# Kernel tuning notes

Hardware: AMD Instinct MI355X
Metric: run time of the kernel (lower is better)

The kernel has to match this reference:

```python
import jax, jax.numpy as jnp
import numpy as np

B = 1024
D = 128  # in_out_dim


def _lin(k, i, o):
    return jax.random.normal(k, (i, o), jnp.float32) / np.sqrt(i)


def setup_inputs() -> dict:
    key = jax.random.key(0)
    ks = jax.random.split(key, 24)
    inp = {
        'pseudo_t': jax.random.uniform(ks[0], (), jnp.float32),
        'x': jax.random.normal(ks[1], (B, D), jnp.float32),
        'g_x': jax.random.normal(ks[2], (B, 1), jnp.float32),
        'p': jax.random.uniform(ks[3], (B, 1), jnp.float32),
        # GRN encoder: 128->1024->960->896 (Tanh), decoder 896->128
        'gw0': _lin(ks[4], 128, 1024), 'gb0': jnp.zeros((1024,), jnp.float32),
        'gw1': _lin(ks[5], 1024, 960), 'gb1': jnp.zeros((960,), jnp.float32),
        'gw2': _lin(ks[6], 960, 896), 'gb2': jnp.zeros((896,), jnp.float32),
        'gdw': _lin(ks[7], 896, 128), 'gdb': jnp.zeros((128,), jnp.float32),
        # BRD encoder: 129->512->448 (Tanh), decoder 448->1
        'bw0': _lin(ks[8], 129, 512), 'bb0': jnp.zeros((512,), jnp.float32),
        'bw1': _lin(ks[9], 512, 448), 'bb1': jnp.zeros((448,), jnp.float32),
        'bdw': _lin(ks[10], 448, 1), 'bdb': jnp.zeros((1,), jnp.float32),
    }
    return inp


def reference(pseudo_t, x, g_x, p, gw0, gb0, gw1, gb1, gw2, gb2, gdw, gdb,
              bw0, bb0, bw1, bb1, bdw, bdb):
    bsz = x.shape[0]
    x_gene = x[:, :-1]                       # [B, D-1]
    s = jnp.full((bsz, 1), pseudo_t, x.dtype)

    def grn(state):                          # [..., D] -> [..., D]
        h = jnp.tanh(state @ gw0 + gb0)
        h = jnp.tanh(h @ gw1 + gb1)
        h = jnp.tanh(h @ gw2 + gb2)
        return h @ gdw + gdb

    dx_dt = grn(jnp.concatenate([s, x_gene], axis=1))   # [B, D]

    # BRD growth function g(x, t)
    st = jnp.concatenate([s, x], axis=1)                # [B, D+1]
    e = jnp.tanh(st @ bw0 + bb0)
    e = jnp.tanh(e @ bw1 + bb1)
    g = e @ bdw + bdb                                   # [B, 1]

    # trace of d(dx_dt[:, :D-1]) / d(x_gene), per sample (CNF divergence)
    s_scalar = jnp.reshape(pseudo_t, (1,)).astype(x.dtype)

    def f_single(xg_i):                                 # [D-1] -> [D]
        return grn(jnp.concatenate([s_scalar, xg_i]))

    jac = jax.vmap(jax.jacfwd(f_single))(x_gene)        # [B, D, D-1]
    tr = jnp.trace(jac[:, :D - 1, :], axis1=1, axis2=2) # [B]

    dp_dt = g - p * tr[:, None]                         # [B, 1]
    return (dx_dt, g, dp_dt)
```

## Files before the change

### kernel.cpp

```cpp
#include <hip/hip_runtime.h>


typedef __bf16 bf16;
typedef __bf16 bf16x8 __attribute__((ext_vector_type(8)));
typedef float floatx4 __attribute__((ext_vector_type(4)));

#if defined(__has_builtin)
#if __has_builtin(__builtin_amdgcn_global_load_lds)
#define HAVE_GLL 1
#endif
#endif

typedef __attribute__((address_space(3))) char lds_char_t;
typedef __attribute__((address_space(1))) const char gbl_char_t;

__device__ inline void async_load16(const void* gp, void* lp) {
#ifdef HAVE_GLL
  __builtin_amdgcn_global_load_lds((gbl_char_t*)gp, (lds_char_t*)lp, 16, 0, 0);
#else
  *(bf16x8*)lp = *(const bf16x8*)gp;
#endif
}

__device__ inline void stage_async(const bf16* src, long row0, int ld, int kc,
                                   bf16* dst, int wid, int sr8, int cph) {
#pragma unroll
  for (int t = 0; t < 4; ++t) {
    const int r = (wid * 4 + t) * 8 + sr8;
    const int csrc = (cph - r) & 7;
    async_load16(src + (row0 + r) * (size_t)ld + kc + csrc * 8,
                 dst + r * 64 + cph * 8);
  }
}

__device__ inline void mfma_block(const bf16* As, const bf16* Bs,
                                  floatx4 (&acc)[4][4], int wm, int wn,
                                  int l16, int quad) {
#pragma unroll
  for (int ks = 0; ks < 2; ++ks) {
    bf16x8 af[4], bfv[4];
#pragma unroll
    for (int mt = 0; mt < 4; ++mt) {
      const int r = wm * 64 + mt * 16 + l16;
      const int c = (ks * 4 + quad + r) & 7;
      af[mt] = *(const bf16x8*)(As + r * 64 + c * 8);
    }
#pragma unroll
    for (int nt = 0; nt < 4; ++nt) {
      const int r = wn * 64 + nt * 16 + l16;
      const int c = (ks * 4 + quad + r) & 7;
      bfv[nt] = *(const bf16x8*)(Bs + r * 64 + c * 8);
    }
#pragma unroll
    for (int mt = 0; mt < 4; ++mt)
#pragma unroll
      for (int nt = 0; nt < 4; ++nt)
        acc[mt][nt] = __builtin_amdgcn_mfma_f32_16x16x32_bf16(af[mt], bfv[nt], acc[mt][nt], 0, 0, 0);
  }
}

struct TArgs {
  const bf16* A;
  const bf16* B;
  const bf16* d1b;
  bf16* Upr;
  const bf16* d2b;
  const float* gdw;
  float* tr;
  int i0; int K; int ch;
};

template <int MODE>
__global__ __launch_bounds__(256, 4) void kt_tile(TArgs p) {
  const int idx = blockIdx.x;
  const int mt8 = (idx >> 3) & 7;
  const int nb  = ((idx >> 6) << 3) + (idx & 7);
  if (nb >= p.ch) return;
  if (MODE == 1 && mt8 == 7) return;

  __shared__ __align__(16) char lds[34816];
  bf16* As = (bf16*)lds;
  bf16* Bs = As + 8192;
  bf16* bounce = (bf16*)lds;
  __shared__ float red4[4];

  const int tid  = threadIdx.x;
  const int wid  = tid >> 6, lane = tid & 63;
  const int wm   = wid & 1, wn = wid >> 1;
  const int quad = lane >> 4, l16 = lane & 15;
  const int sr8  = lane >> 3, cph = lane & 7;
  const int m0   = mt8 * 128;
  const int ig   = p.i0 + nb;
  const int n0   = nb * 128;

  floatx4 acc[4][4];
#pragma unroll
  for (int a = 0; a < 4; ++a)
#pragma unroll
    for (int b = 0; b < 4; ++b)
#pragma unroll
      for (int r = 0; r < 4; ++r) acc[a][b][r] = 0.0f;

  for (int kc = 0; kc < p.K; kc += 64) {
    stage_async(p.A, m0, 1024, kc, As, wid, sr8, cph);
    stage_async(p.B, n0, 1024, kc, Bs, wid, sr8, cph);
    __syncthreads();
    mfma_block(As, Bs, acc, wm, wn, l16, quad);
    __syncthreads();
  }

  if (MODE == 0) {
#pragma unroll
    for (int nt = 0; nt < 4; ++nt) {
      const int nl = wn * 64 + nt * 16 + l16;
#pragma unroll
      for (int mt = 0; mt < 4; ++mt)
#pragma unroll
        for (int r = 0; r < 4; ++r) {
          const int ml = wm * 64 + mt * 16 + quad * 4 + r;
          const int mg = m0 + ml;
          const float d1v = (mg < 960) ? (float)p.d1b[(size_t)ig * 960 + mg] : 0.0f;
          bounce[nl * 136 + ml] = (bf16)(acc[mt][nt][r] * d1v);
        }
    }
    __syncthreads();
    const int r2 = tid >> 1, half16 = tid & 1;
#pragma unroll
    for (int c = 0; c < 8; ++c) {
      const int ch16 = half16 * 8 + c;
      bf16x8 v = *(const bf16x8*)(bounce + r2 * 136 + ch16 * 8);
      *(bf16x8*)(p.Upr + (size_t)(n0 + r2) * 1024 + m0 + ch16 * 8) = v;
    }
  } else {
    float s = 0.0f;
#pragma unroll
    for (int nt = 0; nt < 4; ++nt) {
      const int d = wn * 64 + nt * 16 + l16;
      if (d < 127) {
#pragma unroll
        for (int mt = 0; mt < 4; ++mt)
#pragma unroll
          for (int r = 0; r < 4; ++r) {
            const int mg = m0 + wm * 64 + mt * 16 + quad * 4 + r;
            const float w = (float)p.d2b[(size_t)ig * 896 + mg] * p.gdw[mg * 128 + d];
            s += acc[mt][nt][r] * w;
          }
      }
    }
#pragma unroll
    for (int off = 1; off < 64; off <<= 1) s += __shfl_xor(s, off, 64);
    if (lane == 0) red4[wid] = s;
    __syncthreads();
    if (tid == 0) atomicAdd(p.tr + ig, red4[0] + red4[1] + red4[2] + red4[3]);
  }
}

struct FArgs {
  const bf16* A; int lda;
  const bf16* Bt; int ldb;
  const float* bias;
  bf16* C; int ldc;
  bf16* D; int ldd;
  float* outF; int ldo;
  int K; int realN;
};

template <int ACT>
__global__ __launch_bounds__(256) void kt_fwd(FArgs p) {
  __shared__ __align__(16) bf16 As[8192];
  __shared__ __align__(16) bf16 Bs[8192];
  const int tid  = threadIdx.x;
  const int wid  = tid >> 6, lane = tid & 63;
  const int wm   = wid & 1, wn = wid >> 1;
  const int quad = lane >> 4, l16 = lane & 15;
  const int sr8  = lane >> 3, cph = lane & 7;
  const int m0   = blockIdx.x * 128;
  const int bn0  = blockIdx.y * 128;

  floatx4 acc[4][4];
#pragma unroll
  for (int a = 0; a < 4; ++a)
#pragma unroll
    for (int b = 0; b < 4; ++b)
#pragma unroll
      for (int r = 0; r < 4; ++r) acc[a][b][r] = 0.0f;

  for (int kc = 0; kc < p.K; kc += 64) {
    stage_async(p.A, m0, p.lda, kc, As, wid, sr8, cph);
    stage_async(p.Bt, bn0, p.ldb, kc, Bs, wid, sr8, cph);
    __syncthreads();
    mfma_block(As, Bs, acc, wm, wn, l16, quad);
    __syncthreads();
  }

#pragma unroll
  for (int nt = 0; nt < 4; ++nt) {
    const int ng = bn0 + wn * 64 + nt * 16 + l16;
    const float bv = (ng < p.realN) ? p.bias[ng] : 0.0f;
#pragma unroll
    for (int mt = 0; mt < 4; ++mt)
#pragma unroll
      for (int r = 0; r < 4; ++r) {
        const int i = m0 + wm * 64 + mt * 16 + quad * 4 + r;
        const float v = acc[mt][nt][r] + bv;
        if (ACT) {
          const float t = tanhf(v);
          p.C[(size_t)i * p.ldc + ng] = (ng < p.realN) ? (bf16)t : (bf16)0.0f;
          if (p.D && ng < p.realN)
            p.D[(size_t)i * p.ldd + ng] = (bf16)(1.0f - t * t);
        } else if (ng < p.realN) {
          p.outF[(size_t)i * p.ldo + ng] = v;
        }
      }
  }
}

struct PArgs {
  const float *gw0, *gw1, *gw2, *gdw, *bw0, *bw1, *pt, *x;
  bf16 *gw0b, *gw0t, *gw1t, *gw2t, *gdwt, *bw0t, *bw1t, *Xg, *Xb;
};

__device__ inline void tpose_tile(bf16* dst, const float* src, int R, int C,
                                  int ldd, int tile, int tilesX, float* tl,
                                  int tid) {
  const int r0 = (tile % tilesX) * 64;
  const int c0 = (tile / tilesX) * 64;
  const int tx = tid & 63, ty0 = tid >> 6;
#pragma unroll
  for (int i = 0; i < 16; ++i) {
    const int ty = ty0 + i * 4;
    const int r = r0 + ty, c = c0 + tx;
    tl[ty * 65 + tx] = (r < R && c < C) ? src[(size_t)r * C + c] : 0.0f;
  }
  __syncthreads();
#pragma unroll
  for (int i = 0; i < 16; ++i) {
    const int ty = ty0 + i * 4;
    dst[(size_t)(c0 + ty) * ldd + r0 + tx] = (bf16)tl[tx * 65 + ty];
  }
}

__global__ __launch_bounds__(256) void kt_prep(PArgs p) {
  __shared__ float tl[64 * 65];
  int b = blockIdx.x;
  const int t = threadIdx.x;
  if (b < 512) { p.gw0b[b * 256 + t] = (bf16)p.gw0[b * 256 + t]; return; }
  b -= 512;
  if (b < 768) {
    const int idx = b * 256 + t;
    const int i = idx / 192, c = idx % 192;
    const float s = p.pt[0];
    float vb;
    if (c == 0) vb = s;
    else if (c <= 128) vb = p.x[i * 128 + c - 1];
    else vb = 0.0f;
    p.Xb[i * 192 + c] = (bf16)vb;
    if (c < 128) p.Xg[i * 128 + c] = (bf16)((c == 0) ? s : p.x[i * 128 + c - 1]);
    return;
  }
  b -= 768;
  if (b < 32)  { tpose_tile(p.gw0t, p.gw0, 128, 1024, 128, b, 2, tl, t);  return; }
  b -= 32;
  if (b < 256) { tpose_tile(p.gw1t, p.gw1, 1024, 960, 1024, b, 16, tl, t); return; }
  b -= 256;
  if (b < 256) { tpose_tile(p.gw2t, p.gw2, 960, 896, 1024, b, 16, tl, t); return; }
  b -= 256;
  if (b < 32)  { tpose_tile(p.gdwt, p.gdw, 896, 128, 1024, b, 16, tl, t); return; }
  b -= 32;
  if (b < 24)  { tpose_tile(p.bw0t, p.bw0, 129, 512, 192, b, 3, tl, t);  return; }
  b -= 24;
  if (b < 64)  { tpose_tile(p.bw1t, p.bw1, 512, 448, 512, b, 8, tl, t);  return; }
}

__global__ __launch_bounds__(256) void kt_g0(bf16* G0, const bf16* gw0b,
                                             const bf16* d0b, int i0, int ch) {
  const int b = blockIdx.x;
  const int nb = ((b >> 9) << 3) + (b & 7);
  const int inner = (b >> 3) & 63;
  if (nb >= ch) return;
  const int e = inner * 256 + threadIdx.x;
  const int d = e >> 7;
  const int j = (e & 127) << 3;
  const int ig = i0 + nb;
  const int wsel = (d + 1 < 128) ? d + 1 : 127;
  bf16x8 gv = *(const bf16x8*)(gw0b + wsel * 1024 + j);
  bf16x8 dv = *(const bf16x8*)(d0b + (size_t)ig * 1024 + j);
  bf16x8 v;
#pragma unroll
  for (int k = 0; k < 8; ++k) v[k] = (bf16)((float)gv[k] * (float)dv[k]);
  *(bf16x8*)(G0 + ((size_t)nb * 128 + d) * 1024 + j) = v;
}

__global__ __launch_bounds__(256) void kt_gdot(const bf16* e1b, const float* bdw,
                                               const float* bdb, float* gf, float* gout) {
  const int i = blockIdx.x * 4 + (threadIdx.x >> 6);
  const int lane = threadIdx.x & 63;
  float s = 0.0f;
  for (int k = lane; k < 448; k += 64) s += (float)e1b[(size_t)i * 512 + k] * bdw[k];
#pragma unroll
  for (int off = 32; off > 0; off >>= 1) s += __shfl_down(s, off, 64);
  if (lane == 0) {
    const float v = s + bdb[0];
    gf[i] = v;
    gout[i] = v;
  }
}

__global__ __launch_bounds__(256) void kt_fin(const float* gf, const float* tr,
                                              const float* pp, float* dp) {
  const int i = blockIdx.x * 256 + threadIdx.x;
  if (i < 1024) dp[i] = gf[i] - pp[i] * tr[i];
}

extern "C" void kernel_launch(void* const* d_in, const int* in_sizes, int n_in,
                              void* d_out, int out_size, void* d_ws, size_t ws_size,
                              hipStream_t stream) {
  const float* pt  = (const float*)d_in[0];
  const float* x   = (const float*)d_in[1];
  const float* pp  = (const float*)d_in[3];
  const float* gw0 = (const float*)d_in[4];
  const float* gb0 = (const float*)d_in[5];
  const float* gw1 = (const float*)d_in[6];
  const float* gb1 = (const float*)d_in[7];
  const float* gw2 = (const float*)d_in[8];
  const float* gb2 = (const float*)d_in[9];
  const float* gdw = (const float*)d_in[10];
  const float* gdb = (const float*)d_in[11];
  const float* bw0 = (const float*)d_in[12];
  const float* bb0 = (const float*)d_in[13];
  const float* bw1 = (const float*)d_in[14];
  const float* bb1 = (const float*)d_in[15];
  const float* bdw = (const float*)d_in[16];
  const float* bdb = (const float*)d_in[17];
  float* out = (float*)d_out;

  char* w = (char*)d_ws;
  size_t used = 0;
  auto alloc = [&](size_t nbytes) -> void* {
    void* r = w + used;
    used += (nbytes + 255) & ~(size_t)255;
    return r;
  };
  bf16* gw0b = (bf16*)alloc((size_t)128 * 1024 * 2);
  bf16* gw0t = (bf16*)alloc((size_t)1024 * 128 * 2);
  bf16* gw1t = (bf16*)alloc((size_t)1024 * 1024 * 2);
  bf16* gw2t = (bf16*)alloc((size_t)1024 * 1024 * 2);
  bf16* gdwt = (bf16*)alloc((size_t)128 * 1024 * 2);
  bf16* bw0t = (bf16*)alloc((size_t)512 * 192 * 2);
  bf16* bw1t = (bf16*)alloc((size_t)512 * 512 * 2);
  bf16* Xg   = (bf16*)alloc((size_t)1024 * 128 * 2);
  bf16* Xb   = (bf16*)alloc((size_t)1024 * 192 * 2);
  bf16* h0b  = (bf16*)alloc((size_t)1024 * 1024 * 2);
  bf16* h1b  = (bf16*)alloc((size_t)1024 * 1024 * 2);
  bf16* h2b  = (bf16*)alloc((size_t)1024 * 1024 * 2);
  bf16* e0b  = (bf16*)alloc((size_t)1024 * 512 * 2);
  bf16* e1b  = (bf16*)alloc((size_t)1024 * 512 * 2);
  bf16* d0b  = (bf16*)alloc((size_t)1024 * 1024 * 2);
  bf16* d1b  = (bf16*)alloc((size_t)1024 * 960 * 2);
  bf16* d2b  = (bf16*)alloc((size_t)1024 * 896 * 2);
  float* gf  = (float*)alloc(1024 * 4);
  float* tr  = (float*)alloc(1024 * 4);

  const size_t perSample = (size_t)128 * 1024 * 2;
  size_t avail = (ws_size > used) ? ws_size - used : 0;
  int CH = (int)(avail / (2 * perSample));
  if (CH > 256) CH = 256;
  if (CH < 1) CH = 1;
  bf16* G0  = (bf16*)alloc((size_t)CH * perSample);
  bf16* Upr = (bf16*)(w + used);

  hipMemsetAsync(tr, 0, 1024 * 4, stream);

  {
    PArgs a{gw0, gw1, gw2, gdw, bw0, bw1, pt, x,
            gw0b, gw0t, gw1t, gw2t, gdwt, bw0t, bw1t, Xg, Xb};
    kt_prep<<<dim3(1944), 256, 0, stream>>>(a);
  }

  {
    FArgs a{}; a.A = Xg; a.lda = 128; a.Bt = gw0t; a.ldb = 128; a.bias = gb0;
    a.C = h0b; a.ldc = 1024; a.D = d0b; a.ldd = 1024; a.K = 128; a.realN = 1024;
    kt_fwd<1><<<dim3(8, 8), 256, 0, stream>>>(a);
  }
  {
    FArgs a{}; a.A = h0b; a.lda = 1024; a.Bt = gw1t; a.ldb = 1024; a.bias = gb1;
    a.C = h1b; a.ldc = 1024; a.D = d1b; a.ldd = 960; a.K = 1024; a.realN = 960;
    kt_fwd<1><<<dim3(8, 8), 256, 0, stream>>>(a);
  }
  {
    FArgs a{}; a.A = h1b; a.lda = 1024; a.Bt = gw2t; a.ldb = 1024; a.bias = gb2;
    a.C = h2b; a.ldc = 1024; a.D = d2b; a.ldd = 896; a.K = 1024; a.realN = 896;
    kt_fwd<1><<<dim3(8, 7), 256, 0, stream>>>(a);
  }
  {
    FArgs a{}; a.A = h2b; a.lda = 1024; a.Bt = gdwt; a.ldb = 1024; a.bias = gdb;
    a.outF = out; a.ldo = 128; a.K = 896; a.realN = 128;
    kt_fwd<0><<<dim3(8, 1), 256, 0, stream>>>(a);
  }
  {
    FArgs a{}; a.A = Xb; a.lda = 192; a.Bt = bw0t; a.ldb = 192; a.bias = bb0;
    a.C = e0b; a.ldc = 512; a.K = 192; a.realN = 512;
    kt_fwd<1><<<dim3(8, 4), 256, 0, stream>>>(a);
  }
  {
    FArgs a{}; a.A = e0b; a.lda = 512; a.Bt = bw1t; a.ldb = 512; a.bias = bb1;
    a.C = e1b; a.ldc = 512; a.K = 512; a.realN = 448;
    kt_fwd<1><<<dim3(8, 4), 256, 0, stream>>>(a);
  }
  kt_gdot<<<dim3(256), 256, 0, stream>>>(e1b, bdw, bdb, gf, out + 131072);

  for (int i0 = 0; i0 < 1024; i0 += CH) {
    const int ch = (1024 - i0 < CH) ? (1024 - i0) : CH;
    const int ch8 = (ch + 7) & ~7;
    kt_g0<<<dim3(ch8 * 64), 256, 0, stream>>>(G0, gw0b, d0b, i0, ch);
    {
      TArgs a{}; a.A = gw1t; a.B = G0; a.d1b = d1b; a.Upr = Upr; a.i0 = i0;
      a.K = 1024; a.ch = ch;
      kt_tile<0><<<dim3(8 * ch8), 256, 0, stream>>>(a);
    }
    {
      TArgs a{}; a.A = gw2t; a.B = Upr; a.d2b = d2b; a.gdw = gdw; a.tr = tr;
      a.i0 = i0; a.K = 960; a.ch = ch;
      kt_tile<1><<<dim3(8 * ch8), 256, 0, stream>>>(a);
    }
  }

  kt_fin<<<dim3(4), 256, 0, stream>>>(gf, tr, pp, out + 132096);
}
```

Baseline: 847.2 us.

## Fuse per-sample G0 scaling into tile GEMM operand load, drop kt_g0

Removes the separate kt_g0 kernel that materialized a per-sample scaled copy of gw0 (G0) in global memory. Instead a shifted bf16 copy of gw0 is prepared once in kt_prep, and kt_tile<0> multiplies the B fragments by the per-sample tanh-derivative vector d0b as it loads them from LDS. This saves the G0 write and read traffic, and frees workspace so the chunk size CH can double, giving fewer loop iterations. In exchange it adds per-fragment VALU multiplies and d0b global loads inside the MFMA inner loop.

```diff
diff --git a/kernel.cpp b/kernel.cpp
--- a/kernel.cpp
+++ b/kernel.cpp
@@ -62,6 +62,7 @@
 struct TArgs {
   const bf16* A;
   const bf16* B;
+  const bf16* d0b;
   const bf16* d1b;
   bf16* Upr;
   const bf16* d2b;
@@ -103,9 +104,37 @@
 
   for (int kc = 0; kc < p.K; kc += 64) {
     stage_async(p.A, m0, 1024, kc, As, wid, sr8, cph);
-    stage_async(p.B, n0, 1024, kc, Bs, wid, sr8, cph);
-    __syncthreads();
-    mfma_block(As, Bs, acc, wm, wn, l16, quad);
+    stage_async(p.B, (MODE == 0) ? 0 : n0, 1024, kc, Bs, wid, sr8, cph);
+    __syncthreads();
+#pragma unroll
+    for (int ks = 0; ks < 2; ++ks) {
+      bf16x8 af[4], bfv[4];
+      bf16x8 dv;
+      if (MODE == 0)
+        dv = *(const bf16x8*)(p.d0b + (size_t)ig * 1024 + kc + (ks * 4 + quad) * 8);
+#pragma unroll
+      for (int mt = 0; mt < 4; ++mt) {
+        const int r = wm * 64 + mt * 16 + l16;
+        const int c = (ks * 4 + quad + r) & 7;
+        af[mt] = *(const bf16x8*)(As + r * 64 + c * 8);
+      }
+#pragma unroll
+      for (int nt = 0; nt < 4; ++nt) {
+        const int r = wn * 64 + nt * 16 + l16;
+        const int c = (ks * 4 + quad + r) & 7;
+        bfv[nt] = *(const bf16x8*)(Bs + r * 64 + c * 8);
+        if (MODE == 0) {
+#pragma unroll
+          for (int e = 0; e < 8; ++e)
+            bfv[nt][e] = (bf16)((float)bfv[nt][e] * (float)dv[e]);
+        }
+      }
+#pragma unroll
+      for (int mt = 0; mt < 4; ++mt)
+#pragma unroll
+        for (int nt = 0; nt < 4; ++nt)
+          acc[mt][nt] = __builtin_amdgcn_mfma_f32_16x16x32_bf16(af[mt], bfv[nt], acc[mt][nt], 0, 0, 0);
+    }
     __syncthreads();
   }
 
@@ -217,7 +246,7 @@
 
 struct PArgs {
   const float *gw0, *gw1, *gw2, *gdw, *bw0, *bw1, *pt, *x;
-  bf16 *gw0b, *gw0t, *gw1t, *gw2t, *gdwt, *bw0t, *bw1t, *Xg, *Xb;
+  bf16 *gw0s, *gw0t, *gw1t, *gw2t, *gdwt, *bw0t, *bw1t, *Xg, *Xb;
 };
 
 __device__ inline void tpose_tile(bf16* dst, const float* src, int R, int C,
@@ -244,7 +273,13 @@
   __shared__ float tl[64 * 65];
   int b = blockIdx.x;
   const int t = threadIdx.x;
-  if (b < 512) { p.gw0b[b * 256 + t] = (bf16)p.gw0[b * 256 + t]; return; }
+  if (b < 512) {
+    const int idx = b * 256 + t;
+    const int d = idx >> 10, j = idx & 1023;
+    const int wsel = (d + 1 < 128) ? d + 1 : 127;
+    p.gw0s[idx] = (bf16)p.gw0[wsel * 1024 + j];
+    return;
+  }
   b -= 512;
   if (b < 768) {
     const int idx = b * 256 + t;
@@ -270,25 +305,6 @@
   if (b < 24)  { tpose_tile(p.bw0t, p.bw0, 129, 512, 192, b, 3, tl, t);  return; }
   b -= 24;
   if (b < 64)  { tpose_tile(p.bw1t, p.bw1, 512, 448, 512, b, 8, tl, t);  return; }
-}
-
-__global__ __launch_bounds__(256) void kt_g0(bf16* G0, const bf16* gw0b,
-                                             const bf16* d0b, int i0, int ch) {
-  const int b = blockIdx.x;
-  const int nb = ((b >> 9) << 3) + (b & 7);
-  const int inner = (b >> 3) & 63;
-  if (nb >= ch) return;
-  const int e = inner * 256 + threadIdx.x;
-  const int d = e >> 7;
-  const int j = (e & 127) << 3;
-  const int ig = i0 + nb;
-  const int wsel = (d + 1 < 128) ? d + 1 : 127;
-  bf16x8 gv = *(const bf16x8*)(gw0b + wsel * 1024 + j);
-  bf16x8 dv = *(const bf16x8*)(d0b + (size_t)ig * 1024 + j);
-  bf16x8 v;
-#pragma unroll
-  for (int k = 0; k < 8; ++k) v[k] = (bf16)((float)gv[k] * (float)dv[k]);
-  *(bf16x8*)(G0 + ((size_t)nb * 128 + d) * 1024 + j) = v;
 }
 
 __global__ __launch_bounds__(256) void kt_gdot(const bf16* e1b, const float* bdw,
@@ -341,7 +357,7 @@
     used += (nbytes + 255) & ~(size_t)255;
     return r;
   };
-  bf16* gw0b = (bf16*)alloc((size_t)128 * 1024 * 2);
+  bf16* gw0s = (bf16*)alloc((size_t)128 * 1024 * 2);
   bf16* gw0t = (bf16*)alloc((size_t)1024 * 128 * 2);
   bf16* gw1t = (bf16*)alloc((size_t)1024 * 1024 * 2);
   bf16* gw2t = (bf16*)alloc((size_t)1024 * 1024 * 2);
@@ -363,17 +379,16 @@
 
   const size_t perSample = (size_t)128 * 1024 * 2;
   size_t avail = (ws_size > used) ? ws_size - used : 0;
-  int CH = (int)(avail / (2 * perSample));
+  int CH = (int)(avail / perSample);
   if (CH > 256) CH = 256;
   if (CH < 1) CH = 1;
-  bf16* G0  = (bf16*)alloc((size_t)CH * perSample);
   bf16* Upr = (bf16*)(w + used);
 
   hipMemsetAsync(tr, 0, 1024 * 4, stream);
 
   {
     PArgs a{gw0, gw1, gw2, gdw, bw0, bw1, pt, x,
-            gw0b, gw0t, gw1t, gw2t, gdwt, bw0t, bw1t, Xg, Xb};
+            gw0s, gw0t, gw1t, gw2t, gdwt, bw0t, bw1t, Xg, Xb};
     kt_prep<<<dim3(1944), 256, 0, stream>>>(a);
   }
 
@@ -412,10 +427,9 @@
   for (int i0 = 0; i0 < 1024; i0 += CH) {
     const int ch = (1024 - i0 < CH) ? (1024 - i0) : CH;
     const int ch8 = (ch + 7) & ~7;
-    kt_g0<<<dim3(ch8 * 64), 256, 0, stream>>>(G0, gw0b, d0b, i0, ch);
     {
-      TArgs a{}; a.A = gw1t; a.B = G0; a.d1b = d1b; a.Upr = Upr; a.i0 = i0;
-      a.K = 1024; a.ch = ch;
+      TArgs a{}; a.A = gw1t; a.B = gw0s; a.d0b = d0b; a.d1b = d1b; a.Upr = Upr;
+      a.i0 = i0; a.K = 1024; a.ch = ch;
       kt_tile<0><<<dim3(8 * ch8), 256, 0, stream>>>(a);
     }
     {
```

Result: slower. 994.3 us (+17.4%).
